# Kernel optimization log

Measured on AMD Instinct MI355X. Metric: run time of the kernel, lower is better.

The kernel has to match this reference:

```python
import jax, jax.numpy as jnp
import numpy as np

B, T, C, H = 4, 2048, 768, 12
D = C // H  # head_size = 64
ROPE_BASE = 10000.0


def rotary_tables(seq_len, dim, dtype=jnp.float32):
    # dim = head_size; uses dim//2 frequencies
    inv_freq = 1.0 / (ROPE_BASE ** (jnp.arange(0, dim, 2, dtype=jnp.float32) / dim))
    t = jnp.arange(seq_len, dtype=jnp.float32)
    freqs = jnp.outer(t, inv_freq)  # [T, D/2]
    return jnp.cos(freqs).astype(dtype), jnp.sin(freqs).astype(dtype)


def apply_rotary(x, cos, sin):
    # x: [B, H, T, D]; cos/sin: [T, D/2] broadcast over B,H
    d = x.shape[-1] // 2
    x1, x2 = x[..., :d], x[..., d:]
    y1 = x1 * cos + x2 * sin
    y2 = -x1 * sin + x2 * cos
    return jnp.concatenate([y1, y2], axis=-1)


def setup_inputs() -> dict:
    key = jax.random.key(0)
    ks = jax.random.split(key, 5)
    x = jax.random.normal(ks[0], (B, T, C), dtype=jnp.float32)
    W_attn = jax.random.normal(ks[1], (C, 3 * C), dtype=jnp.float32) * (1.0 / np.sqrt(C))
    b_attn = jax.random.normal(ks[2], (3 * C,), dtype=jnp.float32) * 0.02
    W_proj = jax.random.normal(ks[3], (C, C), dtype=jnp.float32) * (1.0 / np.sqrt(C))
    b_proj = jax.random.normal(ks[4], (C,), dtype=jnp.float32) * 0.02
    return {"x": x, "W_attn": W_attn, "b_attn": b_attn, "W_proj": W_proj, "b_proj": b_proj}


def reference(x, W_attn, b_attn, W_proj, b_proj):
    Bx, Tx, Cx = x.shape
    qkv = x @ W_attn + b_attn  # [B, T, 3C]
    q, k, v = jnp.split(qkv, 3, axis=-1)
    # [B, T, C] -> [B, H, T, D]
    to_heads = lambda a: a.reshape(Bx, Tx, H, D).transpose(0, 2, 1, 3)
    q, k, v = to_heads(q), to_heads(k), to_heads(v)
    cos, sin = rotary_tables(Tx, D, x.dtype)
    q = apply_rotary(q, cos, sin)
    k = apply_rotary(k, cos, sin)
    scale = 1.0 / np.sqrt(D)
    scores = jnp.einsum('bhqd,bhkd->bhqk', q, k) * scale  # [B, H, T, T]
    causal = jnp.tril(jnp.ones((Tx, Tx), dtype=bool))
    scores = jnp.where(causal, scores, jnp.finfo(scores.dtype).min)
    attn = jax.nn.softmax(scores, axis=-1)
    y = jnp.einsum('bhqk,bhkd->bhqd', attn, v)  # [B, H, T, D]
    y = y.transpose(0, 2, 1, 3).reshape(Bx, Tx, Cx)
    return y @ W_proj + b_proj
```

## Files before the change

### kernel.cpp

```cpp
#include <hip/hip_runtime.h>
#include <hip/hip_bf16.h>

#define BB 4
#define TT 2048
#define CC 768
#define HH 12
#define DD 64
#define MM (BB * TT)
#define BH (BB * HH)

typedef __bf16 bf16_t;
typedef __bf16 bf16x8 __attribute__((ext_vector_type(8)));
typedef __bf16 bf16x4 __attribute__((ext_vector_type(4)));
typedef float f32x4 __attribute__((ext_vector_type(4)));
typedef float f32x16 __attribute__((ext_vector_type(16)));

__device__ __forceinline__ float fast_exp2(float x) {
#if __has_builtin(__builtin_amdgcn_exp2f)
    return __builtin_amdgcn_exp2f(x);
#else
    return exp2f(x);
#endif
}

__device__ __forceinline__ uint32_t pk2(float lo, float hi) {
    bf16_t l = (bf16_t)lo, h = (bf16_t)hi;
    uint16_t lu = __builtin_bit_cast(uint16_t, l);
    uint16_t hu = __builtin_bit_cast(uint16_t, h);
    return ((uint32_t)hu << 16) | lu;
}

__device__ __forceinline__ void gload_lds16(const void* g, void* l) {
    __builtin_amdgcn_global_load_lds(
        (const __attribute__((address_space(1))) uint32_t*)g,
        (__attribute__((address_space(3))) uint32_t*)l, 16, 0, 0);
}

__global__ void prep(const float* __restrict__ x,
                     const float* __restrict__ W_attn, const float* __restrict__ W_proj,
                     bf16_t* __restrict__ xb, bf16_t* __restrict__ WaT, bf16_t* __restrict__ WpT,
                     float* __restrict__ trig) {
    int blk = blockIdx.x;
    if (blk < 6144) {
        int tid = blk * 256 + threadIdx.x;
        float4 v = ((const float4*)x)[tid];
        bf16x4 o;
        o[0] = (bf16_t)v.x; o[1] = (bf16_t)v.y; o[2] = (bf16_t)v.z; o[3] = (bf16_t)v.w;
        ((bf16x4*)xb)[tid] = o;
    } else if (blk < 6144 + 1728 + 576) {
        bool isA = blk < 6144 + 1728;
        int blk2 = blk - (isA ? 6144 : 6144 + 1728);
        const float* W = isA ? W_attn : W_proj;
        bf16_t* WT = isA ? WaT : WpT;
        int N = isA ? 2304 : 768;
        int k0 = (blk2 % 24) * 32, n0 = (blk2 / 24) * 32;
        __shared__ bf16_t tile[32][33];
        int tx = threadIdx.x & 31, ty = threadIdx.x >> 5;
#pragma unroll
        for (int r = 0; r < 4; ++r) {
            int kl = ty * 4 + r;
            tile[kl][tx] = (bf16_t)W[(size_t)(k0 + kl) * N + n0 + tx];
        }
        __syncthreads();
#pragma unroll
        for (int r = 0; r < 4; ++r) {
            int nl = ty * 4 + r;
            WT[(size_t)(n0 + nl) * 768 + k0 + tx] = tile[tx][nl];
        }
    } else {
        int e = (blk - (6144 + 1728 + 576)) * 1024 + threadIdx.x * 4;
        int d = e >> 11, t0 = e & 2047;
        float infr = exp2f(-(float)d * 0.4152410118609828f);
#pragma unroll
        for (int r = 0; r < 4; ++r) {
            float fr = (float)(t0 + r) * infr;
            float sn, cs;
            sincosf(fr, &sn, &cs);
            trig[d * 2048 + t0 + r] = cs;
            trig[65536 + d * 2048 + t0 + r] = sn;
        }
    }
}

#define GEMM_CORE(A_, BT_, acc_)                                                       \
    __shared__ bf16_t As[2][128 * 32];                                                 \
    __shared__ bf16_t Bs[2][128 * 32];                                                 \
    int tid = threadIdx.x;                                                             \
    int wv = tid >> 6, lane = tid & 63, c = lane & 15, quad = lane >> 4;               \
    int wm = (wv >> 1) * 64, wn = (wv & 1) * 64;                                       \
    int m0 = blockIdx.x * 128, n0 = blockIdx.y * 128;                                  \
    int srow = wv * 32 + (lane >> 2);                                                  \
    int slot = lane & 3;                                                               \
    auto stage = [&](int buf, int k0) {                                                \
        _Pragma("unroll")                                                              \
        for (int ins = 0; ins < 2; ++ins) {                                            \
            int r = srow + ins * 16;                                                   \
            int g = (slot - ((r >> 1) & 3)) & 3;                                       \
            const bf16_t* ga = A_ + (size_t)(m0 + r) * K + k0 + g * 8;                 \
            const bf16_t* gb = BT_ + (size_t)(n0 + r) * K + k0 + g * 8;                \
            gload_lds16(ga, &As[buf][(wv * 32 + ins * 16) * 32]);                      \
            gload_lds16(gb, &Bs[buf][(wv * 32 + ins * 16) * 32]);                      \
        }                                                                              \
    };                                                                                 \
    int s_rd = (quad + ((c >> 1) & 3)) & 3;                                            \
    const int nk = K / 32;                                                             \
    stage(0, 0);                                                                       \
    for (int kt = 0; kt < nk; ++kt) {                                                  \
        __syncthreads();                                                               \
        if (kt + 1 < nk) stage((kt + 1) & 1, (kt + 1) * 32);                           \
        int buf = kt & 1;                                                              \
        bf16x8 af[4], bfr[4];                                                          \
        _Pragma("unroll")                                                              \
        for (int i = 0; i < 4; ++i) af[i] = *(const bf16x8*)&As[buf][(wm + i * 16 + c) * 32 + s_rd * 8];  \
        _Pragma("unroll")                                                              \
        for (int j = 0; j < 4; ++j) bfr[j] = *(const bf16x8*)&Bs[buf][(wn + j * 16 + c) * 32 + s_rd * 8]; \
        _Pragma("unroll")                                                              \
        for (int i = 0; i < 4; ++i)                                                    \
            _Pragma("unroll")                                                          \
            for (int j = 0; j < 4; ++j)                                                \
                acc_[i][j] = __builtin_amdgcn_mfma_f32_16x16x32_bf16(af[i], bfr[j], acc_[i][j], 0, 0, 0); \
    }

__global__ __launch_bounds__(256, 4) void gemm_qkv(
        const bf16_t* __restrict__ A, const bf16_t* __restrict__ BT,
        const float* __restrict__ bias, const float* __restrict__ trig,
        bf16_t* __restrict__ Qh, bf16_t* __restrict__ Kh, bf16_t* __restrict__ Vt) {
    const int K = 768;
    __shared__ __align__(16) bf16_t smem[17408];
    bf16_t* Asp = smem;
    bf16_t* Bsp = smem + 8192;
    int tid = threadIdx.x;
    int wv = tid >> 6, lane = tid & 63, c = lane & 15, quad = lane >> 4;
    int wm = (wv >> 1) * 64, wn = (wv & 1) * 64;
    int m0 = blockIdx.x * 128, n0 = blockIdx.y * 128;
    int srow = wv * 32 + (lane >> 2);
    int slot = lane & 3;
    auto stage = [&](int buf, int k0) {
#pragma unroll
        for (int ins = 0; ins < 2; ++ins) {
            int r = srow + ins * 16;
            int g = (slot - ((r >> 1) & 3)) & 3;
            gload_lds16(A + (size_t)(m0 + r) * K + k0 + g * 8, &Asp[buf * 4096 + (wv * 32 + ins * 16) * 32]);
            gload_lds16(BT + (size_t)(n0 + r) * K + k0 + g * 8, &Bsp[buf * 4096 + (wv * 32 + ins * 16) * 32]);
        }
    };
    int s_rd = (quad + ((c >> 1) & 3)) & 3;
    f32x4 acc[4][4] = {};
    const int nk = K / 32;
    stage(0, 0);
    for (int kt = 0; kt < nk; ++kt) {
        __syncthreads();
        if (kt + 1 < nk) stage((kt + 1) & 1, (kt + 1) * 32);
        int buf = kt & 1;
        bf16x8 af[4], bfr[4];
#pragma unroll
        for (int i = 0; i < 4; ++i) af[i] = *(const bf16x8*)&Asp[buf * 4096 + (wm + i * 16 + c) * 32 + s_rd * 8];
#pragma unroll
        for (int j = 0; j < 4; ++j) bfr[j] = *(const bf16x8*)&Bsp[buf * 4096 + (wn + j * 16 + c) * 32 + s_rd * 8];
#pragma unroll
        for (int i = 0; i < 4; ++i)
#pragma unroll
            for (int j = 0; j < 4; ++j)
                acc[i][j] = __builtin_amdgcn_mfma_f32_16x16x32_bf16(af[i], bfr[j], acc[i][j], 0, 0, 0);
    }
    __syncthreads();

    int type = n0 / 768;
    int hloc = ((n0 % 768) + wn) >> 6;
    int bidx = m0 >> 11;
    int colb = n0 + wn;
    int tb = (m0 + wm) & (TT - 1);
    bf16_t* epi = smem + wv * 4352;
    int rrow = lane >> 3, cchunk = lane & 7;

    if (type < 2) {
        const float rscale = (type == 0) ? 0.125f * 1.44269504088896f : 1.0f;
#pragma unroll
        for (int j = 0; j < 2; ++j) {
            int dlo = j * 16 + c;
            const float* ctab = trig + dlo * 2048 + tb;
            const float* stab = trig + 65536 + dlo * 2048 + tb;
            float blo = bias[colb + j * 16 + c];
            float bhi = bias[colb + (j + 2) * 16 + c];
#pragma unroll
            for (int i = 0; i < 4; ++i) {
                f32x4 cs4 = *(const f32x4*)(ctab + i * 16 + quad * 4);
                f32x4 sn4 = *(const f32x4*)(stab + i * 16 + quad * 4);
#pragma unroll
                for (int r = 0; r < 4; ++r) {
                    int lr = i * 16 + quad * 4 + r;
                    float a = acc[i][j][r] + blo;
                    float b2 = acc[i][j + 2][r] + bhi;
                    epi[lr * 68 + dlo]      = (bf16_t)((a * cs4[r] + b2 * sn4[r]) * rscale);
                    epi[lr * 68 + dlo + 32] = (bf16_t)((-a * sn4[r] + b2 * cs4[r]) * rscale);
                }
            }
        }
        bf16_t* dst = (type == 0 ? Qh : Kh) + (size_t)(bidx * HH + hloc) * TT * DD + (size_t)tb * DD;
#pragma unroll
        for (int it = 0; it < 8; ++it) {
            int row = it * 8 + rrow;
            bf16x8 v = *(const bf16x8*)&epi[row * 68 + cchunk * 8];
            *(bf16x8*)&dst[row * 64 + cchunk * 8] = v;
        }
    } else {
        int kt64 = tb >> 6;
#pragma unroll
        for (int j = 0; j < 4; ++j) {
            int dim = j * 16 + c;
            float bv = bias[colb + j * 16 + c];
            int rot = (dim & 7) * 8;
#pragma unroll
            for (int i = 0; i < 4; ++i)
#pragma unroll
                for (int r = 0; r < 4; ++r) {
                    int tin = i * 16 + quad * 4 + r;
                    epi[dim * 68 + ((tin + rot) & 63)] = (bf16_t)(acc[i][j][r] + bv);
                }
        }
        bf16_t* dstV = Vt + (size_t)(bidx * HH + hloc) * (TT / 64) * 4096 + (size_t)kt64 * 4096;
#pragma unroll
        for (int it = 0; it < 8; ++it) {
            int dim = it * 8 + rrow;
            int src = ((cchunk + (dim & 7)) & 7) * 8;
            bf16x8 v = *(const bf16x8*)&epi[dim * 68 + src];
            *(bf16x8*)&dstV[dim * 64 + cchunk * 8] = v;
        }
    }
}

__global__ __launch_bounds__(256, 4) void gemm_proj(
        const bf16_t* __restrict__ A, const bf16_t* __restrict__ BT,
        const float* __restrict__ bias, float* __restrict__ Cout) {
    const int K = 768;
    f32x4 acc[4][4] = {};
    GEMM_CORE(A, BT, acc)
#pragma unroll
    for (int j = 0; j < 4; ++j) {
        int col = n0 + wn + j * 16 + c;
        float bv = bias[col];
#pragma unroll
        for (int i = 0; i < 4; ++i) {
            int row = m0 + wm + i * 16 + quad * 4;
#pragma unroll
            for (int r = 0; r < 4; ++r)
                Cout[(size_t)(row + r) * CC + col] = acc[i][j][r] + bv;
        }
    }
}

__constant__ signed char RK_QT[20] = {11,10,9,8,15,15,7,14,14,13,13,6,12,12,5,4,3,2,1,0};
__constant__ signed char RK_PC[20] = { 2, 2,2,2, 0, 1,2, 0, 1, 0, 1,2, 0, 1,2,2,2,2,2,2};

__global__ __launch_bounds__(256, 3) void flash_attn(
        const bf16_t* __restrict__ Q, const bf16_t* __restrict__ Kc,
        const bf16_t* __restrict__ Vt, bf16_t* __restrict__ Y,
        float* __restrict__ Opart, float* __restrict__ Lpart) {
    __shared__ __align__(16) bf16_t smem[22016];
    bf16_t* KsB = smem;
    bf16_t* VsB = smem + 13824;

    int blk = blockIdx.x;
    int xcd = blk & 7, j = blk >> 3;
    int r = j / 6, bh = xcd * 6 + (j - r * 6);
    int qt = RK_QT[r], pc = RK_PC[r];
    int kt0 = (pc == 1) ? (qt + 1) : 0;
    int ktend = (pc == 0) ? (qt + 1) : (2 * qt + 2);
    int nct = ktend - kt0;

    int wv = threadIdx.x >> 6, lane = threadIdx.x & 63;
    int b = bh / HH, h = bh - b * HH;
    int q31 = lane & 31, hi = lane >> 5;
    int qbw = qt * 128 + wv * 32;
    const bf16_t* Qg = Q + ((size_t)bh * TT + qbw) * DD;
    const bf16_t* Kg = Kc + (size_t)bh * TT * DD;
    const bf16_t* Vg = Vt + (size_t)bh * (TT / 64) * 4096;

    bf16x8 qf[4];
#pragma unroll
    for (int dk = 0; dk < 4; ++dk)
        qf[dk] = *(const bf16x8*)(Qg + (size_t)q31 * DD + dk * 16 + hi * 8);

    int srow = wv * 16 + (lane >> 3);
    int slot = lane & 7;
    auto stage = [&](int buf, int kt64) {
#pragma unroll
        for (int ins = 0; ins < 2; ++ins) {
            int rr = srow + ins * 8;
            int g = (slot - (rr & 7)) & 7;
            gload_lds16(Kg + (size_t)(kt64 * 64 + rr) * 64 + g * 8, &KsB[buf * 4096 + (wv * 16 + ins * 8) * 64]);
            gload_lds16(Vg + (size_t)kt64 * 4096 + rr * 64 + g * 8, &VsB[buf * 4096 + (wv * 16 + ins * 8) * 64]);
        }
    };

    f32x16 O[2] = {};
    float lsum = 0.0f;

    stage(0, kt0);

#define FA_TILE(FULL)                                                                   \
    {                                                                                   \
        int kt = kt0 + i;                                                               \
        int buf = i & 1;                                                                \
        __syncthreads();                                                                \
        if (i + 1 < nct) stage((i + 1) & 1, kt + 1);                                    \
        _Pragma("unroll")                                                               \
        for (int t32 = 0; t32 < 2; ++t32) {                                             \
            int ks = kt * 64 + t32 * 32;                                                \
            if (!(FULL) && ks > qbw) continue;                                          \
            bool masked = !(FULL) && (ks == qbw);                                       \
            f32x16 st = {};                                                             \
            __builtin_amdgcn_s_setprio(1);                                              \
            _Pragma("unroll")                                                           \
            for (int dk = 0; dk < 4; ++dk) {                                            \
                int row = t32 * 32 + q31;                                               \
                int sl = ((dk * 2 + hi) + (row & 7)) & 7;                               \
                bf16x8 kf = *(const bf16x8*)&KsB[buf * 4096 + row * 64 + sl * 8];       \
                st = __builtin_amdgcn_mfma_f32_32x32x16_bf16(kf, qf[dk], st, 0, 0, 0);  \
            }                                                                           \
            __builtin_amdgcn_s_setprio(0);                                              \
            bf16x8 vf[2][2];                                                            \
            _Pragma("unroll")                                                           \
            for (int dt = 0; dt < 2; ++dt)                                              \
                _Pragma("unroll")                                                       \
                for (int sli = 0; sli < 2; ++sli) {                                     \
                    int row = dt * 32 + q31;                                            \
                    int ch = t32 * 4 + sli * 2 + hi;                                    \
                    int sl = (ch + (row & 7)) & 7;                                      \
                    vf[dt][sli] = *(const bf16x8*)&VsB[buf * 4096 + row * 64 + sl * 8]; \
                }                                                                       \
            float p[16];                                                                \
            _Pragma("unroll")                                                           \
            for (int rr = 0; rr < 16; ++rr) {                                           \
                float e = fast_exp2(st[rr]);                                            \
                if (masked) {                                                           \
                    int keyl = (rr & 3) + 8 * (rr >> 2) + 4 * hi;                       \
                    if (keyl > q31) e = 0.0f;                                           \
                }                                                                       \
                p[rr] = e;                                                              \
            }                                                                           \
            lsum += ((((p[0] + p[1]) + (p[2] + p[3])) + ((p[4] + p[5]) + (p[6] + p[7])))\
                  + (((p[8] + p[9]) + (p[10] + p[11])) + ((p[12] + p[13]) + (p[14] + p[15])))); \
            union { uint32_t u[4]; bf16x8 v; } pb[2];                                   \
            _Pragma("unroll")                                                           \
            for (int sli = 0; sli < 2; ++sli) {                                         \
                uint32_t a0 = pk2(p[sli * 8 + 0], p[sli * 8 + 1]);                      \
                uint32_t b0 = pk2(p[sli * 8 + 2], p[sli * 8 + 3]);                      \
                uint32_t a1 = pk2(p[sli * 8 + 4], p[sli * 8 + 5]);                      \
                uint32_t b1 = pk2(p[sli * 8 + 6], p[sli * 8 + 7]);                      \
                asm("v_permlane32_swap_b32 %0, %1" : "+v"(a0), "+v"(a1));               \
                asm("v_permlane32_swap_b32 %0, %1" : "+v"(b0), "+v"(b1));               \
                pb[sli].u[0] = a0; pb[sli].u[1] = b0; pb[sli].u[2] = a1; pb[sli].u[3] = b1; \
            }                                                                           \
            __builtin_amdgcn_s_setprio(1);                                              \
            _Pragma("unroll")                                                           \
            for (int dt = 0; dt < 2; ++dt) {                                            \
                O[dt] = __builtin_amdgcn_mfma_f32_32x32x16_bf16(vf[dt][0], pb[0].v, O[dt], 0, 0, 0); \
                O[dt] = __builtin_amdgcn_mfma_f32_32x32x16_bf16(vf[dt][1], pb[1].v, O[dt], 0, 0, 0); \
            }                                                                           \
            __builtin_amdgcn_s_setprio(0);                                              \
        }                                                                               \
    }

    int nfull = 2 * qt - kt0;
    if (nfull > nct) nfull = nct;
    if (nfull < 0) nfull = 0;
    int i = 0;
    for (; i < nfull; ++i) FA_TILE(1)
    for (; i < nct; ++i) FA_TILE(0)
#undef FA_TILE

    float l = lsum;
    l += __shfl_xor(l, 32);

    if (pc == 2) {
        float inv_l = 1.0f / l;
        int row = b * TT + qbw + q31;
#pragma unroll
        for (int dt = 0; dt < 2; ++dt)
#pragma unroll
            for (int g = 0; g < 4; ++g) {
                bf16x4 ov;
#pragma unroll
                for (int rr = 0; rr < 4; ++rr) ov[rr] = (bf16_t)(O[dt][g * 4 + rr] * inv_l);
                *(bf16x4*)(Y + (size_t)row * CC + h * DD + dt * 32 + g * 8 + hi * 4) = ov;
            }
    } else {
        int pslot = bh * 4 + (qt - 12);
        int idx = pslot * 2 + pc;
        float* Op = Opart + ((size_t)idx * 128 + wv * 32 + q31) * 64;
#pragma unroll
        for (int dt = 0; dt < 2; ++dt)
#pragma unroll
            for (int g = 0; g < 4; ++g) {
                f32x4 ov;
#pragma unroll
                for (int rr = 0; rr < 4; ++rr) ov[rr] = O[dt][g * 4 + rr];
                *(f32x4*)(Op + dt * 32 + g * 8 + hi * 4) = ov;
            }
        if (hi == 0) Lpart[idx * 128 + wv * 32 + q31] = l;
    }
}

__global__ __launch_bounds__(256, 4) void combine_partials(
        const float* __restrict__ Opart, const float* __restrict__ Lpart,
        bf16_t* __restrict__ Y) {
    int pslot = blockIdx.x;
    int bh = pslot >> 2, qt = 12 + (pslot & 3);
    int b = bh / HH, h = bh - b * HH;
    int t = threadIdx.x;
    int q = t >> 1, dh = (t & 1) * 32;
    const float* p0 = Opart + ((size_t)(pslot * 2 + 0) * 128 + q) * 64 + dh;
    const float* p1 = Opart + ((size_t)(pslot * 2 + 1) * 128 + q) * 64 + dh;
    float inv = 1.0f / (Lpart[(pslot * 2 + 0) * 128 + q] + Lpart[(pslot * 2 + 1) * 128 + q]);
    bf16_t* y = Y + ((size_t)(b * TT + qt * 128 + q)) * CC + h * DD + dh;
#pragma unroll
    for (int g = 0; g < 4; ++g) {
        f32x4 a = *(const f32x4*)(p0 + g * 8);
        f32x4 a2 = *(const f32x4*)(p0 + g * 8 + 4);
        f32x4 c = *(const f32x4*)(p1 + g * 8);
        f32x4 c2 = *(const f32x4*)(p1 + g * 8 + 4);
        bf16x8 o;
#pragma unroll
        for (int rr = 0; rr < 4; ++rr) o[rr] = (bf16_t)((a[rr] + c[rr]) * inv);
#pragma unroll
        for (int rr = 0; rr < 4; ++rr) o[4 + rr] = (bf16_t)((a2[rr] + c2[rr]) * inv);
        *(bf16x8*)(y + g * 8) = o;
    }
}

extern "C" void kernel_launch(void* const* d_in, const int* in_sizes, int n_in,
                              void* d_out, int out_size, void* d_ws, size_t ws_size,
                              hipStream_t stream) {
    const float* x      = (const float*)d_in[0];
    const float* W_attn = (const float*)d_in[1];
    const float* b_attn = (const float*)d_in[2];
    const float* W_proj = (const float*)d_in[3];
    const float* b_proj = (const float*)d_in[4];
    float* out = (float*)d_out;

    unsigned char* ws = (unsigned char*)d_ws;
    size_t off = 0;
    auto alloc = [&](size_t bytes) { void* p = ws + off; off += (bytes + 255) & ~(size_t)255; return p; };
    bf16_t* xb  = (bf16_t*)alloc((size_t)MM * CC * 2);
    bf16_t* WaT = (bf16_t*)alloc((size_t)3 * CC * CC * 2);
    bf16_t* WpT = (bf16_t*)alloc((size_t)CC * CC * 2);
    bf16_t* Qh  = (bf16_t*)alloc((size_t)BH * TT * DD * 2);
    bf16_t* Kh  = (bf16_t*)alloc((size_t)BH * TT * DD * 2);
    bf16_t* Vt  = (bf16_t*)alloc((size_t)BH * TT * DD * 2);
    bf16_t* Yb  = (bf16_t*)alloc((size_t)MM * CC * 2);
    float*  Opart = (float*)alloc((size_t)192 * 2 * 128 * 64 * 4);
    float*  Lpart = (float*)alloc((size_t)192 * 2 * 128 * 4);
    float*  trig  = (float*)alloc((size_t)2 * 32 * 2048 * 4);

    prep<<<dim3(6144 + 1728 + 576 + 64), 256, 0, stream>>>(x, W_attn, W_proj, xb, WaT, WpT, trig);
    gemm_qkv<<<dim3(MM / 128, 3 * CC / 128), 256, 0, stream>>>(xb, WaT, b_attn, trig, Qh, Kh, Vt);
    flash_attn<<<dim3(960), 256, 0, stream>>>(Qh, Kh, Vt, Yb, Opart, Lpart);
    combine_partials<<<dim3(192), 256, 0, stream>>>(Opart, Lpart, Yb);
    gemm_proj<<<dim3(MM / 128, CC / 128), 256, 0, stream>>>(Yb, WpT, b_proj, out);
}
```

Measured before the change: 189.6 us.

## Load K/V fragments directly from global memory instead of LDS staging

Drops the double-buffered LDS staging of K and V tiles in the flash attention kernel, along with its per-tile barriers. Each wave now reads its K and V MFMA fragments straight from global memory into registers. Occupancy hint is raised from 3 to 4 blocks per CU, since no shared memory is used. This removes LDS traffic and synchronisation, but all four waves re-read the same K/V data from global/L2 with no prefetch overlap, so load latency is exposed.

Result: slower. 307.5 us (+62.2%).

```diff
diff --git a/kernel.cpp b/kernel.cpp
--- a/kernel.cpp
+++ b/kernel.cpp
@@ -252,14 +252,10 @@
 __constant__ signed char RK_QT[20] = {11,10,9,8,15,15,7,14,14,13,13,6,12,12,5,4,3,2,1,0};
 __constant__ signed char RK_PC[20] = { 2, 2,2,2, 0, 1,2, 0, 1, 0, 1,2, 0, 1,2,2,2,2,2,2};
 
-__global__ __launch_bounds__(256, 3) void flash_attn(
+__global__ __launch_bounds__(256, 4) void flash_attn(
         const bf16_t* __restrict__ Q, const bf16_t* __restrict__ Kc,
         const bf16_t* __restrict__ Vt, bf16_t* __restrict__ Y,
         float* __restrict__ Opart, float* __restrict__ Lpart) {
-    __shared__ __align__(16) bf16_t smem[22016];
-    bf16_t* KsB = smem;
-    bf16_t* VsB = smem + 13824;
-
     int blk = blockIdx.x;
     int xcd = blk & 7, j = blk >> 3;
     int r = j / 6, bh = xcd * 6 + (j - r * 6);
@@ -281,54 +277,34 @@
     for (int dk = 0; dk < 4; ++dk)
         qf[dk] = *(const bf16x8*)(Qg + (size_t)q31 * DD + dk * 16 + hi * 8);
 
-    int srow = wv * 16 + (lane >> 3);
-    int slot = lane & 7;
-    auto stage = [&](int buf, int kt64) {
-#pragma unroll
-        for (int ins = 0; ins < 2; ++ins) {
-            int rr = srow + ins * 8;
-            int g = (slot - (rr & 7)) & 7;
-            gload_lds16(Kg + (size_t)(kt64 * 64 + rr) * 64 + g * 8, &KsB[buf * 4096 + (wv * 16 + ins * 8) * 64]);
-            gload_lds16(Vg + (size_t)kt64 * 4096 + rr * 64 + g * 8, &VsB[buf * 4096 + (wv * 16 + ins * 8) * 64]);
-        }
-    };
-
     f32x16 O[2] = {};
     float lsum = 0.0f;
-
-    stage(0, kt0);
 
 #define FA_TILE(FULL)                                                                   \
     {                                                                                   \
         int kt = kt0 + i;                                                               \
-        int buf = i & 1;                                                                \
-        __syncthreads();                                                                \
-        if (i + 1 < nct) stage((i + 1) & 1, kt + 1);                                    \
         _Pragma("unroll")                                                               \
         for (int t32 = 0; t32 < 2; ++t32) {                                             \
             int ks = kt * 64 + t32 * 32;                                                \
             if (!(FULL) && ks > qbw) continue;                                          \
             bool masked = !(FULL) && (ks == qbw);                                       \
+            const bf16_t* Kt = Kg + (size_t)(kt * 64 + t32 * 32 + q31) * 64;            \
+            const bf16_t* Vb = Vg + (size_t)kt * 4096 + (size_t)q31 * 64;               \
+            bf16x8 kfr[4], vf[2][2];                                                    \
+            _Pragma("unroll")                                                           \
+            for (int dk = 0; dk < 4; ++dk)                                              \
+                kfr[dk] = *(const bf16x8*)(Kt + dk * 16 + hi * 8);                      \
+            _Pragma("unroll")                                                           \
+            for (int dt = 0; dt < 2; ++dt)                                              \
+                _Pragma("unroll")                                                       \
+                for (int sli = 0; sli < 2; ++sli)                                       \
+                    vf[dt][sli] = *(const bf16x8*)(Vb + dt * 2048 + t32 * 32 + sli * 16 + hi * 8); \
             f32x16 st = {};                                                             \
             __builtin_amdgcn_s_setprio(1);                                              \
             _Pragma("unroll")                                                           \
-            for (int dk = 0; dk < 4; ++dk) {                                            \
-                int row = t32 * 32 + q31;                                               \
-                int sl = ((dk * 2 + hi) + (row & 7)) & 7;                               \
-                bf16x8 kf = *(const bf16x8*)&KsB[buf * 4096 + row * 64 + sl * 8];       \
-                st = __builtin_amdgcn_mfma_f32_32x32x16_bf16(kf, qf[dk], st, 0, 0, 0);  \
-            }                                                                           \
+            for (int dk = 0; dk < 4; ++dk)                                              \
+                st = __builtin_amdgcn_mfma_f32_32x32x16_bf16(kfr[dk], qf[dk], st, 0, 0, 0); \
             __builtin_amdgcn_s_setprio(0);                                              \
-            bf16x8 vf[2][2];                                                            \
-            _Pragma("unroll")                                                           \
-            for (int dt = 0; dt < 2; ++dt)                                              \
-                _Pragma("unroll")                                                       \
-                for (int sli = 0; sli < 2; ++sli) {                                     \
-                    int row = dt * 32 + q31;                                            \
-                    int ch = t32 * 4 + sli * 2 + hi;                                    \
-                    int sl = (ch + (row & 7)) & 7;                                      \
-                    vf[dt][sli] = *(const bf16x8*)&VsB[buf * 4096 + row * 64 + sl * 8]; \
-                }                                                                       \
             float p[16];                                                                \
             _Pragma("unroll")                                                           \
             for (int rr = 0; rr < 16; ++rr) {                                           \
```
